# Kernel tuning notes

Measured on AMD Instinct MI355X. Metric: run time of the kernel, lower is better.

## Reference

```python
import jax, jax.numpy as jnp
import numpy as np

B, L, D = 16384, 6, 256
LN_EPS = 1e-5


def _layernorm(x, gamma, beta):
    mu = jnp.mean(x, axis=-1, keepdims=True)
    var = jnp.mean(jnp.square(x - mu), axis=-1, keepdims=True)
    return (x - mu) * jax.lax.rsqrt(var + LN_EPS) * gamma + beta


def _mlp_block(x, W, b, ln_g, ln_b):
    # Linear(D, D) -> LayerNorm(D) -> ReLU
    return jax.nn.relu(_layernorm(x @ W + b, ln_g, ln_b))


def setup_inputs() -> dict:
    key = jax.random.key(0)
    ks = jax.random.split(key, 8)
    s = 1.0 / np.sqrt(D)
    return {
        "gfeat": jax.random.normal(ks[0], (B, L, D), jnp.float32),
        "pfeat": jax.random.normal(ks[1], (B, L, D), jnp.float32),
        "Wg": jax.random.normal(ks[2], (D, D), jnp.float32) * s,
        "bg": jax.random.normal(ks[3], (D,), jnp.float32) * s,
        "g_ln_g": jnp.ones((D,), jnp.float32),
        "g_ln_b": jnp.zeros((D,), jnp.float32),
        "Wp": jax.random.normal(ks[4], (D, D), jnp.float32) * s,
        "bp": jax.random.normal(ks[5], (D,), jnp.float32) * s,
        "p_ln_g": jnp.ones((D,), jnp.float32),
        "p_ln_b": jnp.zeros((D,), jnp.float32),
        "wa_g": jax.random.normal(ks[6], (D,), jnp.float32) * s,
        "ba_g": jnp.zeros((), jnp.float32),
        "wa_p": jax.random.normal(ks[7], (D,), jnp.float32) * s,
        "ba_p": jnp.zeros((), jnp.float32),
    }


def reference(gfeat, pfeat, Wg, bg, g_ln_g, g_ln_b, Wp, bp, p_ln_g, p_ln_b,
              wa_g, ba_g, wa_p, ba_p):
    # g_align, p_align: [B, L, D]
    g_align = _mlp_block(gfeat, Wg, bg, g_ln_g, g_ln_b)
    p_align = _mlp_block(pfeat, Wp, bp, p_ln_g, p_ln_b)

    # Original torch code materializes atten[b,l,i,j] = g_align[b,l,i] * p_align[b,l,j]
    # ([B,L,D,D]) then applies Linear(D,1)+sigmoid along j (geno) / along i (path).
    # Mathematically:
    #   geno_att[b,l,i] = sigmoid(g_align[b,l,i] * (p_align[b,l] @ wa_g) + ba_g)
    #   path_att[b,l,j] = sigmoid(p_align[b,l,j] * (g_align[b,l] @ wa_p) + ba_p)
    # so we compute the bilinear reduction without forming the 4D tensor.
    p_red = jnp.einsum('bld,d->bl', p_align, wa_g)[..., None]  # [B,L,1]
    g_red = jnp.einsum('bld,d->bl', g_align, wa_p)[..., None]  # [B,L,1]
    geno_att = jax.nn.sigmoid(g_align * p_red + ba_g)
    path_att = jax.nn.sigmoid(p_align * g_red + ba_p)

    interaction = p_align * path_att + g_align * geno_att  # [B,L,D]
    return interaction
```

## Files before the change

kernel.cpp:

```cpp
#include <hip/hip_runtime.h>
#include <hip/hip_bf16.h>


typedef float f32x4 __attribute__((ext_vector_type(4)));
typedef short short8 __attribute__((ext_vector_type(8)));
typedef unsigned int u32;

#define D_DIM 256
#define ROWS 16
#define NW 4

union S8 { short8 s; u32 u[4]; };

__device__ __forceinline__ u32 f2bfu(float x) {
  u32 u = __float_as_uint(x);
  return (u + 0x7FFFu + ((u >> 16) & 1u)) >> 16;
}
__device__ __forceinline__ float sigm(float x) { return 1.0f / (1.0f + __expf(-x)); }

__device__ __forceinline__ u32 pk2c(float a, float b) {
  __hip_bfloat162 h = __float22bfloat162_rn(float2{a, b});
  union { __hip_bfloat162 h; u32 u; } cv;
  cv.h = h;
  return cv.u;
}

__global__ __launch_bounds__(256) void pack_w_kernel(const float* __restrict__ Wg,
                                                     const float* __restrict__ Wp,
                                                     unsigned short* __restrict__ outp) {
  int b = blockIdx.x;
  const float* W = (b < 32) ? Wg : Wp;
  unsigned short* o = outp + (b < 32 ? 0 : 65536);
  int chunk = (b & 31) * 256 + threadIdx.x;
  int c = chunk >> 9;
  int rest = chunk & 511;
  int t = rest >> 6;
  int l = rest & 63;
  int m = c * 16 + (l & 15);
  int kb = t * 32 + ((l >> 4) << 3);
  short8 v;
#pragma unroll
  for (int j = 0; j < 8; ++j) v[j] = (short)f2bfu(W[(kb + j) * 256 + m]);
  *(short8*)(o + (size_t)chunk * 8) = v;
}


__device__ __forceinline__ void stage_dma(const float* __restrict__ src, float* lbuf,
                                          int w, int lane) {
#pragma unroll
  for (int j = 0; j < 4; ++j) {
    int r = w * 4 + j;
    const float* gp = src + r * D_DIM + ((lane ^ (r & 7)) << 2);
    float* lp = lbuf + r * D_DIM;
    __builtin_amdgcn_global_load_lds(
        (const __attribute__((address_space(1))) u32*)gp,
        (__attribute__((address_space(3))) u32*)lp, 16, 0, 0);
  }
}

__device__ __forceinline__ void barrier_fence() {
  __builtin_amdgcn_s_barrier();
  asm volatile("" ::: "memory");
}

__device__ __forceinline__ short8 readAf32(const float* buf, int t, int lane) {
  const int cl = lane & 15, kg = lane >> 4;
  const int r = cl;
  const int s = r & 7;
  const int c16 = t * 8 + kg * 2;
  const char* base = (const char*)buf + r * 1024;
  float4 x = *(const float4*)(base + ((c16 ^ s) << 4));
  float4 y = *(const float4*)(base + (((c16 + 1) ^ s) << 4));
  S8 rr;
  rr.u[0] = pk2c(x.x, x.y);
  rr.u[1] = pk2c(x.z, x.w);
  rr.u[2] = pk2c(y.x, y.y);
  rr.u[3] = pk2c(y.z, y.w);
  return rr.s;
}

__device__ __forceinline__ void gemm4(f32x4 acc[4], const float* buf,
                                      const short8* __restrict__ wb, int lane, int w) {
  const int bbase = w * 2048 + lane;
#pragma unroll
  for (int h = 0; h < 2; ++h) {
    short8 a[4];
#pragma unroll
    for (int tt = 0; tt < 4; ++tt) a[tt] = readAf32(buf, h * 4 + tt, lane);
#pragma unroll
    for (int c = 0; c < 4; ++c) {
      short8 bf[4];
#pragma unroll
      for (int tt = 0; tt < 4; ++tt) bf[tt] = wb[bbase + c * 512 + (h * 4 + tt) * 64];
#pragma unroll
      for (int tt = 0; tt < 4; ++tt)
        acc[c] = __builtin_amdgcn_mfma_f32_16x16x32_bf16(a[tt], bf[tt], acc[c], 0, 0, 0);
    }
  }
}

__device__ __forceinline__ void statsPhase(f32x4 acc[4], const float* __restrict__ bias,
                                           float smSum[NW][ROWS], float smSq[NW][ROWS],
                                           int lane, int w) {
  float bv[4];
#pragma unroll
  for (int c = 0; c < 4; ++c) bv[c] = bias[w * 64 + c * 16 + (lane & 15)];
#pragma unroll
  for (int r = 0; r < 4; ++r) {
    float s = 0.f, qq = 0.f;
#pragma unroll
    for (int c = 0; c < 4; ++c) {
      float y = acc[c][r] + bv[c];
      acc[c][r] = y;
      s += y; qq += y * y;
    }
#pragma unroll
    for (int m = 1; m < 16; m <<= 1) {
      s += __shfl_xor(s, m, 64);
      qq += __shfl_xor(qq, m, 64);
    }
    if ((lane & 15) == 0) {
      int row = ((lane >> 4) << 2) + r;
      smSum[w][row] = s;
      smSq[w][row] = qq;
    }
  }
}

__device__ __forceinline__ void applyPhase(f32x4 acc[4], f32x4 outAl[4],
                                           const float* __restrict__ gam, const float* __restrict__ bet,
                                           const float* __restrict__ wa,
                                           const float smSum[NW][ROWS], const float smSq[NW][ROWS],
                                           float smRed[NW][ROWS], int lane, int w) {
  int cb = w * 64 + (lane & 15);
  float gv[4], tv[4], wv[4];
#pragma unroll
  for (int c = 0; c < 4; ++c) {
    gv[c] = gam[cb + c * 16];
    tv[c] = bet[cb + c * 16];
    wv[c] = wa[cb + c * 16];
  }
#pragma unroll
  for (int r = 0; r < 4; ++r) {
    int row = ((lane >> 4) << 2) + r;
    float s = 0.f, qq = 0.f;
#pragma unroll
    for (int k = 0; k < NW; ++k) { s += smSum[k][row]; qq += smSq[k][row]; }
    float mu = s * (1.0f / 256.0f);
    float var = fmaxf(qq * (1.0f / 256.0f) - mu * mu, 0.0f);
    float rs = rsqrtf(var + 1e-5f);
    float dp = 0.f;
#pragma unroll
    for (int c = 0; c < 4; ++c) {
      float a = (acc[c][r] - mu) * rs * gv[c] + tv[c];
      a = fmaxf(a, 0.0f);
      outAl[c][r] = a;
      dp += a * wv[c];
    }
#pragma unroll
    for (int m = 1; m < 16; m <<= 1) dp += __shfl_xor(dp, m, 64);
    if ((lane & 15) == 0) smRed[w][row] = dp;
  }
}

__global__ __launch_bounds__(256, 4) void fused_main(
    const float* __restrict__ gfeat, const float* __restrict__ pfeat,
    const float* __restrict__ bg, const float* __restrict__ glng, const float* __restrict__ glnb,
    const float* __restrict__ bp, const float* __restrict__ plng, const float* __restrict__ plnb,
    const float* __restrict__ wag, const float* __restrict__ bag,
    const float* __restrict__ wap, const float* __restrict__ bap,
    const unsigned short* __restrict__ wpk,
    float* __restrict__ outp)
{
  __shared__ float bufA[ROWS * D_DIM];
  __shared__ float smSum[NW][ROWS], smSq[NW][ROWS], smRedG[NW][ROWS], smRedP[NW][ROWS];

  const int tid = threadIdx.x;
  const int lane = tid & 63;
  const int w = tid >> 6;
  const size_t row0 = (size_t)blockIdx.x * ROWS;

  const short8* wbg = (const short8*)wpk;
  const short8* wbp = (const short8*)(wpk + 65536);

  stage_dma(gfeat + row0 * D_DIM, bufA, w, lane);
  asm volatile("s_waitcnt vmcnt(0)" ::: "memory");
  barrier_fence();

  f32x4 accG[4];
#pragma unroll
  for (int c = 0; c < 4; ++c) accG[c] = {0.f, 0.f, 0.f, 0.f};
  gemm4(accG, bufA, wbg, lane, w);
  statsPhase(accG, bg, smSum, smSq, lane, w);
  asm volatile("s_waitcnt lgkmcnt(0)" ::: "memory");
  barrier_fence();

  stage_dma(pfeat + row0 * D_DIM, bufA, w, lane);

  f32x4 alignG[4];
  applyPhase(accG, alignG, glng, glnb, wap, smSum, smSq, smRedG, lane, w);
  asm volatile("s_waitcnt vmcnt(0) lgkmcnt(0)" ::: "memory");
  barrier_fence();

  f32x4 accP[4];
#pragma unroll
  for (int c = 0; c < 4; ++c) accP[c] = {0.f, 0.f, 0.f, 0.f};
  gemm4(accP, bufA, wbp, lane, w);
  statsPhase(accP, bp, smSum, smSq, lane, w);
  asm volatile("s_waitcnt lgkmcnt(0)" ::: "memory");
  barrier_fence();

  applyPhase(accP, accP, plng, plnb, wag, smSum, smSq, smRedP, lane, w);
  asm volatile("s_waitcnt lgkmcnt(0)" ::: "memory");
  barrier_fence();

  const float vbag = bag[0], vbap = bap[0];
#pragma unroll
  for (int r = 0; r < 4; ++r) {
    int row = ((lane >> 4) << 2) + r;
    float gr = 0.f, pr = 0.f;
#pragma unroll
    for (int k = 0; k < NW; ++k) { gr += smRedG[k][row]; pr += smRedP[k][row]; }
    float* orow = outp + (row0 + row) * D_DIM + w * 64 + (lane & 15);
#pragma unroll
    for (int c = 0; c < 4; ++c) {
      float ga = alignG[c][r];
      float pa = accP[c][r];
      float geno = sigm(ga * pr + vbag);
      float path = sigm(pa * gr + vbap);
      orow[c * 16] = pa * path + ga * geno;
    }
  }
}

extern "C" void kernel_launch(void* const* d_in, const int* in_sizes, int n_in,
                              void* d_out, int out_size, void* d_ws, size_t ws_size,
                              hipStream_t stream) {
  const float* gfeat = (const float*)d_in[0];
  const float* pfeat = (const float*)d_in[1];
  const float* Wg   = (const float*)d_in[2];
  const float* bg   = (const float*)d_in[3];
  const float* glng = (const float*)d_in[4];
  const float* glnb = (const float*)d_in[5];
  const float* Wp   = (const float*)d_in[6];
  const float* bp   = (const float*)d_in[7];
  const float* plng = (const float*)d_in[8];
  const float* plnb = (const float*)d_in[9];
  const float* wag  = (const float*)d_in[10];
  const float* bag  = (const float*)d_in[11];
  const float* wap  = (const float*)d_in[12];
  const float* bap  = (const float*)d_in[13];
  float* outp = (float*)d_out;
  unsigned short* wpk = (unsigned short*)d_ws;

  hipLaunchKernelGGL(pack_w_kernel, dim3(64), dim3(256), 0, stream, Wg, Wp, wpk);

  int nrows = in_sizes[0] / D_DIM;
  int nblocks = nrows / ROWS;
  hipLaunchKernelGGL(fused_main, dim3(nblocks), dim3(256), 0, stream,
                     gfeat, pfeat, bg, glng, glnb, bp, plng, plnb,
                     wag, bag, wap, bap, wpk, outp);
}
```

Baseline: 128.0 us.

## Process four row tiles per block with triple-buffered async staging

Each block now handles four 16-row tiles in a loop and keeps three LDS buffers. The next tile's gfeat and pfeat loads are issued while the current tile's GEMMs and layernorm run, with partial vmcnt waits. This aims to hide global-load latency behind compute and to amortize block launch overhead. In exchange, LDS use rises from 16KB to 48KB per block and the grid shrinks fourfold, which lowers occupancy and may rely on the stage_dma vmcnt counts being exactly right.

```diff
diff --git a/kernel.cpp b/kernel.cpp
--- a/kernel.cpp
+++ b/kernel.cpp
@@ -9,6 +9,7 @@
 #define D_DIM 256
 #define ROWS 16
 #define NW 4
+#define TPB 4
 
 union S8 { short8 s; u32 u[4]; };
 
@@ -24,6 +25,11 @@
   cv.h = h;
   return cv.u;
 }
+
+#define WAITV0 asm volatile("s_waitcnt vmcnt(0)" ::: "memory")
+#define WAITV4 asm volatile("s_waitcnt vmcnt(4)" ::: "memory")
+#define WAITV8 asm volatile("s_waitcnt vmcnt(8)" ::: "memory")
+#define WAITL  asm volatile("s_waitcnt lgkmcnt(0)" ::: "memory")
 
 __global__ __launch_bounds__(256) void pack_w_kernel(const float* __restrict__ Wg,
                                                      const float* __restrict__ Wp,
@@ -172,63 +178,81 @@
     const unsigned short* __restrict__ wpk,
     float* __restrict__ outp)
 {
-  __shared__ float bufA[ROWS * D_DIM];
+  __shared__ float bufs[3][ROWS * D_DIM];
   __shared__ float smSum[NW][ROWS], smSq[NW][ROWS], smRedG[NW][ROWS], smRedP[NW][ROWS];
 
   const int tid = threadIdx.x;
   const int lane = tid & 63;
   const int w = tid >> 6;
-  const size_t row0 = (size_t)blockIdx.x * ROWS;
+  const size_t base_row = (size_t)blockIdx.x * TPB * ROWS;
 
   const short8* wbg = (const short8*)wpk;
   const short8* wbp = (const short8*)(wpk + 65536);
-
-  stage_dma(gfeat + row0 * D_DIM, bufA, w, lane);
-  asm volatile("s_waitcnt vmcnt(0)" ::: "memory");
-  barrier_fence();
-
-  f32x4 accG[4];
-#pragma unroll
-  for (int c = 0; c < 4; ++c) accG[c] = {0.f, 0.f, 0.f, 0.f};
-  gemm4(accG, bufA, wbg, lane, w);
-  statsPhase(accG, bg, smSum, smSq, lane, w);
-  asm volatile("s_waitcnt lgkmcnt(0)" ::: "memory");
-  barrier_fence();
-
-  stage_dma(pfeat + row0 * D_DIM, bufA, w, lane);
-
-  f32x4 alignG[4];
-  applyPhase(accG, alignG, glng, glnb, wap, smSum, smSq, smRedG, lane, w);
-  asm volatile("s_waitcnt vmcnt(0) lgkmcnt(0)" ::: "memory");
-  barrier_fence();
-
-  f32x4 accP[4];
-#pragma unroll
-  for (int c = 0; c < 4; ++c) accP[c] = {0.f, 0.f, 0.f, 0.f};
-  gemm4(accP, bufA, wbp, lane, w);
-  statsPhase(accP, bp, smSum, smSq, lane, w);
-  asm volatile("s_waitcnt lgkmcnt(0)" ::: "memory");
-  barrier_fence();
-
-  applyPhase(accP, accP, plng, plnb, wag, smSum, smSq, smRedP, lane, w);
-  asm volatile("s_waitcnt lgkmcnt(0)" ::: "memory");
-  barrier_fence();
-
   const float vbag = bag[0], vbap = bap[0];
-#pragma unroll
-  for (int r = 0; r < 4; ++r) {
-    int row = ((lane >> 4) << 2) + r;
-    float gr = 0.f, pr = 0.f;
-#pragma unroll
-    for (int k = 0; k < NW; ++k) { gr += smRedG[k][row]; pr += smRedP[k][row]; }
-    float* orow = outp + (row0 + row) * D_DIM + w * 64 + (lane & 15);
-#pragma unroll
-    for (int c = 0; c < 4; ++c) {
-      float ga = alignG[c][r];
-      float pa = accP[c][r];
-      float geno = sigm(ga * pr + vbag);
-      float path = sigm(pa * gr + vbap);
-      orow[c * 16] = pa * path + ga * geno;
+
+  stage_dma(gfeat + base_row * D_DIM, bufs[0], w, lane);
+  stage_dma(pfeat + base_row * D_DIM, bufs[1], w, lane);
+
+#pragma unroll
+  for (int i = 0; i < TPB; ++i) {
+    const size_t row0 = base_row + (size_t)i * ROWS;
+    float* bG = bufs[(2 * i) % 3];
+    float* bP = bufs[(2 * i + 1) % 3];
+    float* bGn = bufs[(2 * i + 2) % 3];
+    float* bPn = bufs[(2 * i) % 3];
+
+    if (i + 1 < TPB) {
+      stage_dma(gfeat + (row0 + ROWS) * D_DIM, bGn, w, lane);
+      WAITV8;
+    } else {
+      WAITV4;
+    }
+    barrier_fence();
+
+    f32x4 accG[4];
+#pragma unroll
+    for (int c = 0; c < 4; ++c) accG[c] = {0.f, 0.f, 0.f, 0.f};
+    gemm4(accG, bG, wbg, lane, w);
+    statsPhase(accG, bg, smSum, smSq, lane, w);
+    WAITL;
+    barrier_fence();
+
+    f32x4 alignG[4];
+    applyPhase(accG, alignG, glng, glnb, wap, smSum, smSq, smRedG, lane, w);
+    if (i + 1 < TPB) WAITV4; else WAITV0;
+    WAITL;
+    barrier_fence();
+
+    if (i + 1 < TPB)
+      stage_dma(pfeat + (row0 + ROWS) * D_DIM, bPn, w, lane);
+
+    f32x4 accP[4];
+#pragma unroll
+    for (int c = 0; c < 4; ++c) accP[c] = {0.f, 0.f, 0.f, 0.f};
+    gemm4(accP, bP, wbp, lane, w);
+    statsPhase(accP, bp, smSum, smSq, lane, w);
+    WAITL;
+    barrier_fence();
+
+    applyPhase(accP, accP, plng, plnb, wag, smSum, smSq, smRedP, lane, w);
+    WAITL;
+    barrier_fence();
+
+#pragma unroll
+    for (int r = 0; r < 4; ++r) {
+      int row = ((lane >> 4) << 2) + r;
+      float gr = 0.f, pr = 0.f;
+#pragma unroll
+      for (int k = 0; k < NW; ++k) { gr += smRedG[k][row]; pr += smRedP[k][row]; }
+      float* orow = outp + (row0 + row) * D_DIM + w * 64 + (lane & 15);
+#pragma unroll
+      for (int c = 0; c < 4; ++c) {
+        float ga = alignG[c][r];
+        float pa = accP[c][r];
+        float geno = sigm(ga * pr + vbag);
+        float path = sigm(pa * gr + vbap);
+        orow[c * 16] = pa * path + ga * geno;
+      }
     }
   }
 }
@@ -256,7 +280,7 @@
   hipLaunchKernelGGL(pack_w_kernel, dim3(64), dim3(256), 0, stream, Wg, Wp, wpk);
 
   int nrows = in_sizes[0] / D_DIM;
-  int nblocks = nrows / ROWS;
+  int nblocks = nrows / (ROWS * TPB);
   hipLaunchKernelGGL(fused_main, dim3(nblocks), dim3(256), 0, stream,
                      gfeat, pfeat, bg, glng, glnb, bp, plng, plnb,
                      wag, bag, wap, bap, wpk, outp);
```

Result: slower. 239.6 us (+87.2%).
